# Kernel optimization log

Hardware: AMD Instinct MI355X
Metric: run time of the kernel (lower is better)

Reference implementation:

```python
import jax, jax.numpy as jnp
import numpy as np

BETA = 0.25
COMMIT_W = 1.0
EPS = 1e-6
N_E, E_DIM, C = 8192, 256, 256
B, H, W = 16, 32, 32


def setup_inputs() -> dict:
    key = jax.random.key(0)
    k1, k2, k3 = jax.random.split(key, 3)
    z = jax.random.normal(k1, (B, C, H, W), jnp.float32)
    frozen_codebook = jax.random.normal(k2, (N_E, E_DIM), jnp.float32) * (E_DIM ** -0.5)
    w_transform = jax.random.normal(k3, (C, E_DIM), jnp.float32) * (E_DIM ** -0.5)
    return {"z": z, "frozen_codebook": frozen_codebook, "w_transform": w_transform}


def _rotate_to(src, tgt):
    # Rotation trick: Householder-style rotation of src onto direction of tgt.
    sg = jax.lax.stop_gradient
    norm_src = jnp.linalg.norm(src, axis=-1, keepdims=True)
    norm_tgt = jnp.linalg.norm(tgt, axis=-1, keepdims=True)
    u = src / jnp.clip(norm_src, EPS)          # normalized source
    q = tgt / jnp.clip(norm_tgt, EPS)          # normalized target
    w = u + q
    w = sg(w / jnp.clip(jnp.linalg.norm(w, axis=-1, keepdims=True), EPS))
    u = sg(u)
    q = sg(q)
    e = src  # gradients flow through e only (rotation matrix is detached)
    rotated = (e
               - 2.0 * jnp.sum(e * w, axis=-1, keepdims=True) * w
               + 2.0 * jnp.sum(e * u, axis=-1, keepdims=True) * q)
    return rotated * sg(norm_tgt / jnp.clip(norm_src, EPS))


def reference(z, frozen_codebook, w_transform):
    z = z.astype(jnp.float32)
    zc = jnp.transpose(z, (0, 2, 3, 1))          # b h w c
    z_flat = zc.reshape(-1, zc.shape[-1])        # [N, C]
    codebook = frozen_codebook @ w_transform.T   # [n_e, C] (Linear, no bias)

    # squared L2 distances, argmin under no_grad
    d = (jnp.sum(z_flat ** 2, axis=1, keepdims=True)
         + jnp.sum(codebook ** 2, axis=1)
         - 2.0 * jnp.einsum('bd,nd->bn', z_flat, codebook))
    indices = jnp.argmin(jax.lax.stop_gradient(d), axis=1)  # [N]

    z_q_flat = codebook[indices]                 # [N, C]
    sg = jax.lax.stop_gradient
    loss = (jnp.mean((sg(z_flat) - z_q_flat) ** 2)
            + BETA * jnp.mean((z_flat - sg(z_q_flat)) ** 2)) * COMMIT_W

    z_q_flat = _rotate_to(z_flat, z_q_flat)      # rotation trick
    z_q = z_q_flat.reshape(zc.shape)             # b h w c
    z_q = jnp.transpose(z_q, (0, 3, 1, 2))       # b c h w
    return z_q, loss, indices
```

## Files before the change

kernel.cpp:

```cpp
#include <hip/hip_runtime.h>
#include <math.h>

typedef unsigned short u16;
typedef unsigned int   u32;

#define B_   16
#define C_   256
#define HW_  1024
#define N_   16384
#define NE_  8192
#define K_   256
#define NSPLIT 8
#define CPS  1024
#define NZQ  4194304

typedef _Float16 f16x8 __attribute__((ext_vector_type(8)));
typedef float    f32x16 __attribute__((ext_vector_type(16)));


__device__ __forceinline__ u16 f2h(float x) {
    union { _Float16 h; u16 u; } c;
    c.h = (_Float16)x;
    return c.u;
}

__global__ void k_transpose_z(const float* __restrict__ z, float* __restrict__ zf,
                              u16* __restrict__ zh) {
    __shared__ float tile[32][33];
    int b   = blockIdx.z;
    int hw0 = blockIdx.x * 32;
    int c0  = blockIdx.y * 32;
    int tx = threadIdx.x;
    int ty = threadIdx.y;
    #pragma unroll
    for (int i = 0; i < 4; ++i) {
        int c = c0 + ty + i * 8;
        tile[ty + i * 8][tx] = z[((size_t)b * C_ + c) * HW_ + hw0 + tx];
    }
    __syncthreads();
    #pragma unroll
    for (int i = 0; i < 4; ++i) {
        int hw = hw0 + ty + i * 8;
        size_t o = ((size_t)b * HW_ + hw) * C_ + c0 + tx;
        float v = tile[tx][ty + i * 8];
        zf[o] = v;
        zh[o] = f2h(v);
    }
}

__global__ __launch_bounds__(256) void k_codebook_gemm(
        const float* __restrict__ f, const float* __restrict__ w,
        float* __restrict__ cb, u16* __restrict__ cbh) {
    __shared__ float Fs[16][68];
    __shared__ float Ws[16][68];
    int n0 = blockIdx.x * 64;
    int c0 = blockIdx.y * 64;
    int tid = threadIdx.x;
    int tx = tid & 15, ty = tid >> 4;
    int nl = tid >> 2;
    int kq = (tid & 3) * 4;
    float acc[4][4] = {};
    for (int kb = 0; kb < K_; kb += 16) {
        float4 fv = *(const float4*)&f[(size_t)(n0 + nl) * K_ + kb + kq];
        float4 wv = *(const float4*)&w[(size_t)(c0 + nl) * K_ + kb + kq];
        __syncthreads();
        Fs[kq + 0][nl] = fv.x; Fs[kq + 1][nl] = fv.y; Fs[kq + 2][nl] = fv.z; Fs[kq + 3][nl] = fv.w;
        Ws[kq + 0][nl] = wv.x; Ws[kq + 1][nl] = wv.y; Ws[kq + 2][nl] = wv.z; Ws[kq + 3][nl] = wv.w;
        __syncthreads();
        #pragma unroll
        for (int k = 0; k < 16; ++k) {
            float4 a = *(float4*)&Fs[k][ty * 4];
            float4 b = *(float4*)&Ws[k][tx * 4];
            float av[4] = {a.x, a.y, a.z, a.w};
            float bv[4] = {b.x, b.y, b.z, b.w};
            #pragma unroll
            for (int i = 0; i < 4; ++i)
                #pragma unroll
                for (int j = 0; j < 4; ++j)
                    acc[i][j] += av[i] * bv[j];
        }
    }
    #pragma unroll
    for (int i = 0; i < 4; ++i) {
        size_t o = (size_t)(n0 + ty * 4 + i) * K_ + c0 + tx * 4;
        *(float4*)&cb[o] = make_float4(acc[i][0], acc[i][1], acc[i][2], acc[i][3]);
        *(ushort4*)&cbh[o] = make_ushort4(f2h(acc[i][0]), f2h(acc[i][1]),
                                          f2h(acc[i][2]), f2h(acc[i][3]));
    }
}

__global__ void k_c2(const float* __restrict__ cb, float* __restrict__ c2,
                     double* __restrict__ c2d) {
    int row  = blockIdx.x * 4 + (threadIdx.x >> 6);
    int lane = threadIdx.x & 63;
    float4 v = *(const float4*)&cb[(size_t)row * K_ + lane * 4];
    double s = (double)v.x * v.x + (double)v.y * v.y
             + (double)v.z * v.z + (double)v.w * v.w;
    #pragma unroll
    for (int off = 32; off; off >>= 1) s += __shfl_down(s, off, 64);
    if (lane == 0) { c2d[row] = s; c2[row] = (float)(s * 4096.0 + 262144.0); }
}

__device__ __forceinline__ void ld_lds16(const void* g, void* l) {
    __builtin_amdgcn_global_load_lds((const __attribute__((address_space(1))) void*)g,
                                     (__attribute__((address_space(3))) void*)l, 16, 0, 0);
}

#define INS(M1, M2, U) { u32 t_ = min(M1, U); u32 h_ = max(M1, U); M1 = t_; M2 = min(M2, h_); }

#define SCORE16(ACC, M1, M2, CGBASE, C2B) do {                                    \
    u32 ib_ = (u32)(code0 + (CGBASE));                                            \
    _Pragma("unroll")                                                             \
    for (int h = 0; h < 4; ++h) {                                                 \
        float4 cv = *(const float4*)&(C2B)[(CGBASE) + 8 * h];                     \
        u32 u0 = (((u32)fmaf(-8192.f, (ACC)[4*h+0], cv.x)) << 13) + ib_ + 8*h + 0; \
        u32 u1 = (((u32)fmaf(-8192.f, (ACC)[4*h+1], cv.y)) << 13) + ib_ + 8*h + 1; \
        u32 u2 = (((u32)fmaf(-8192.f, (ACC)[4*h+2], cv.z)) << 13) + ib_ + 8*h + 2; \
        u32 u3 = (((u32)fmaf(-8192.f, (ACC)[4*h+3], cv.w)) << 13) + ib_ + 8*h + 3; \
        INS(M1, M2, u0); INS(M1, M2, u1); INS(M1, M2, u2); INS(M1, M2, u3);       \
    }                                                                             \
} while (0)

#define WAITVM(N) { asm volatile("s_waitcnt vmcnt(" #N ")" ::: "memory"); \
                    __builtin_amdgcn_s_barrier();                          \
                    __builtin_amdgcn_sched_barrier(0); }

__global__ __launch_bounds__(256, 2) void k_scan_mfma(
        const u16* __restrict__ zh, const u16* __restrict__ cbh,
        const float* __restrict__ c2, int* __restrict__ t2i) {
    __shared__ __align__(16) u16 sA[4][8192];
    __shared__ __align__(16) float c2s[1024];

    int r0    = blockIdx.x * 128;
    int split = blockIdx.y;
    int tid  = threadIdx.x;
    int wave = tid >> 6, lane = tid & 63;
    int l31 = lane & 31, q = lane >> 5;
    int ra = ((wave & 1) << 6) + l31;

    const u16* zp = zh + (size_t)(r0 + ((wave >> 1) << 6) + l31) * K_ + q * 8;
    f16x8 zr0[16], zr1[16];
    #pragma unroll
    for (int t = 0; t < 16; ++t) {
        zr0[t] = *(const f16x8*)&zp[t * 16];
        zr1[t] = *(const f16x8*)&zp[32 * K_ + t * 16];
    }

    size_t ga[4]; u32 la[4];
    #pragma unroll
    for (int it = 0; it < 4; ++it) {
        int S = (it * 4 + wave) * 64 + lane;
        int row = S >> 3, u = S & 7;
        ga[it] = (size_t)row * K_ + (u ^ (row & 7)) * 8;
        la[it] = (u32)(it * 4 + wave) * 512;
    }

    u32 m1a = 0xFFFFFFFFu, m2a = 0xFFFFFFFFu;
    u32 m1b = 0xFFFFFFFFu, m2b = 0xFFFFFFFFu;

    const u16* cb0 = cbh + (size_t)split * CPS * K_;

    auto STAGE = [&](int s) {
        const u16* Ab = cb0 + (size_t)(s >> 2) * (128 * K_) + (s & 3) * 64;
        u16* d = &sA[s & 3][0];
        #pragma unroll
        for (int it = 0; it < 4; ++it) ld_lds16(Ab + ga[it], d + la[it]);
    };

    f32x16 acc0 = (f32x16){}, acc1 = (f32x16){}, acc2 = (f32x16){}, acc3 = (f32x16){};

    auto COMPUTE = [&](int ct, int kb) {
        const u16* sAb = &sA[kb][0];
        __builtin_amdgcn_s_setprio(1);
        #pragma unroll
        for (int ks = 0; ks < 4; ++ks) {
            u32 u8 = (u32)(((ks * 2 + q) ^ (l31 & 7)) * 8);
            f16x8 af0 = *(const f16x8*)&sAb[(u32)ra * 64 + u8];
            f16x8 af1 = *(const f16x8*)&sAb[(u32)ra * 64 + 2048 + u8];
            acc0 = __builtin_amdgcn_mfma_f32_32x32x16_f16(af0, zr0[kb * 4 + ks], acc0, 0, 0, 0);
            acc1 = __builtin_amdgcn_mfma_f32_32x32x16_f16(af1, zr0[kb * 4 + ks], acc1, 0, 0, 0);
            acc2 = __builtin_amdgcn_mfma_f32_32x32x16_f16(af0, zr1[kb * 4 + ks], acc2, 0, 0, 0);
            acc3 = __builtin_amdgcn_mfma_f32_32x32x16_f16(af1, zr1[kb * 4 + ks], acc3, 0, 0, 0);
        }
        __builtin_amdgcn_s_setprio(0);
        if (kb == 3) {
            int code0 = split * CPS + ct * 128;
            const float* C2B = &c2s[ct * 128];
            int cga = ((wave & 1) << 6) + (q << 2);
            int cgb = cga + 32;
            SCORE16(acc0, m1a, m2a, cga, C2B);
            SCORE16(acc1, m1a, m2a, cgb, C2B);
            SCORE16(acc2, m1b, m2b, cga, C2B);
            SCORE16(acc3, m1b, m2b, cgb, C2B);
            acc0 = (f32x16){}; acc1 = (f32x16){}; acc2 = (f32x16){}; acc3 = (f32x16){};
        }
    };

    STAGE(0); STAGE(1);
    ld_lds16(&c2[split * CPS + wave * 256 + lane * 4], &c2s[wave * 256]);
    asm volatile("s_waitcnt vmcnt(0)" ::: "memory");
    __builtin_amdgcn_s_barrier();
    __builtin_amdgcn_sched_barrier(0);

    for (int ct = 0; ct < 7; ++ct) {
        #pragma unroll
        for (int kb = 0; kb < 4; ++kb) {
            STAGE(ct * 4 + kb + 2);
            WAITVM(8);
            COMPUTE(ct, kb);
        }
    }
    STAGE(30); WAITVM(8); COMPUTE(7, 0);
    STAGE(31); WAITVM(8); COMPUTE(7, 1);
    WAITVM(4);            COMPUTE(7, 2);
    WAITVM(0);            COMPUTE(7, 3);

    {
        u32 o1 = __shfl_xor(m1a, 32, 64), o2 = __shfl_xor(m2a, 32, 64);
        u32 h = max(m1a, o1); m1a = min(m1a, o1); m2a = min(min(m2a, o2), h);
        o1 = __shfl_xor(m1b, 32, 64); o2 = __shfl_xor(m2b, 32, 64);
        h = max(m1b, o1); m1b = min(m1b, o1); m2b = min(min(m2b, o2), h);
    }
    u32* mbuf = (u32*)&sA[0][0];
    if (q == 0) {
        int base = ((wave * 2 + 0) * 32 + l31) * 2;
        mbuf[base] = m1a; mbuf[base + 1] = m2a;
        base = ((wave * 2 + 1) * 32 + l31) * 2;
        mbuf[base] = m1b; mbuf[base + 1] = m2b;
    }
    __syncthreads();
    if (tid < 128) {
        int zr = tid, wp = zr >> 6, zg = (zr >> 5) & 1, l = zr & 31;
        int iA = (((wp * 2 + 0) * 2 + zg) * 32 + l) * 2;
        int iB = (((wp * 2 + 1) * 2 + zg) * 32 + l) * 2;
        u32 a1 = mbuf[iA], a2 = mbuf[iA + 1];
        u32 b1 = mbuf[iB], b2 = mbuf[iB + 1];
        u32 h  = max(a1, b1), f1 = min(a1, b1);
        u32 f2 = min(min(a2, b2), h);
        size_t o = ((size_t)split * N_ + (r0 + zr)) * 2;
        t2i[o] = (int)(f1 & 0x1FFFu);
        t2i[o + 1] = (int)(f2 & 0x1FFFu);
    }
}

__global__ __launch_bounds__(256) void k_finalize(
        const float* __restrict__ zf, const float* __restrict__ cb,
        const double* __restrict__ c2d, const int* __restrict__ t2i,
        float* __restrict__ out, float* __restrict__ partials) {
    __shared__ int   bidx[16];
    __shared__ float wsum[4];
    __shared__ float tile[16][260];
    int n0 = blockIdx.x * 16;
    int tid = threadIdx.x;
    int wv = tid >> 6, lane = tid & 63;
    int h = lane >> 5, l5 = lane & 31;

    for (int rr = 0; rr < 4; ++rr) {
        int n = n0 + wv * 4 + rr;
        double bs = 1e300; int bi = 0x7fffffff;
        for (int p = 0; p < 8; ++p) {
            int t = 2 * p + h;
            int sp = t >> 1, wsel = t & 1;
            int ci = t2i[((size_t)sp * N_ + n) * 2 + wsel];
            double acc = 0.0;
            const float* zp = zf + (size_t)n * K_;
            const float* cp = cb + (size_t)ci * K_;
            #pragma unroll
            for (int jj = 0; jj < 2; ++jj) {
                float4 zv = *(const float4*)&zp[l5 * 4 + jj * 128];
                float4 cv = *(const float4*)&cp[l5 * 4 + jj * 128];
                acc += (double)zv.x * cv.x + (double)zv.y * cv.y
                     + (double)zv.z * cv.z + (double)zv.w * cv.w;
            }
            #pragma unroll
            for (int off = 1; off < 32; off <<= 1) acc += __shfl_xor(acc, off, 32);
            double sc = c2d[ci] - 2.0 * acc;
            double so = __shfl_xor(sc, 32, 64);
            int    io = __shfl_xor(ci, 32, 64);
            double s0 = h ? so : sc;  int i0 = h ? io : ci;
            double s1 = h ? sc : so;  int i1 = h ? ci : io;
            if (s0 < bs || (s0 == bs && i0 < bi)) { bs = s0; bi = i0; }
            if (s1 < bs || (s1 == bs && i1 < bi)) { bs = s1; bi = i1; }
        }
        if (lane == 0) {
            bidx[wv * 4 + rr] = bi;
            out[(size_t)NZQ + 1 + n] = (float)bi;
        }
    }
    __syncthreads();

    float accl = 0.f;
    for (int l = 0; l < 16; ++l) {
        int n = n0 + l;
        int bi = bidx[l];
        float zq = cb[(size_t)bi * K_ + tid];
        float d  = zf[(size_t)n * K_ + tid] - zq;
        accl += d * d;
        tile[l][tid] = zq;
    }
    #pragma unroll
    for (int off = 32; off; off >>= 1) accl += __shfl_down(accl, off, 64);
    if ((tid & 63) == 0) wsum[tid >> 6] = accl;
    __syncthreads();
    if (tid == 0) partials[blockIdx.x] = wsum[0] + wsum[1] + wsum[2] + wsum[3];
    int b = n0 >> 10, hw0 = n0 & 1023;
    #pragma unroll
    for (int g = 0; g < 4; ++g) {
        float4 v = make_float4(tile[g * 4 + 0][tid], tile[g * 4 + 1][tid],
                               tile[g * 4 + 2][tid], tile[g * 4 + 3][tid]);
        *(float4*)&out[((size_t)b * C_ + tid) * HW_ + hw0 + g * 4] = v;
    }
}

__global__ void k_loss(const float* __restrict__ partials, float* __restrict__ out) {
    __shared__ double ws4[4];
    int tid = threadIdx.x;
    double s = 0.0;
    for (int i = tid; i < 1024; i += 256) s += (double)partials[i];
    #pragma unroll
    for (int off = 32; off; off >>= 1) s += __shfl_down(s, off, 64);
    if ((tid & 63) == 0) ws4[tid >> 6] = s;
    __syncthreads();
    if (tid == 0) {
        double tot = ws4[0] + ws4[1] + ws4[2] + ws4[3];
        out[NZQ] = (float)(1.25 * tot / (double)NZQ);
    }
}

extern "C" void kernel_launch(void* const* d_in, const int* in_sizes, int n_in,
                              void* d_out, int out_size, void* d_ws, size_t ws_size,
                              hipStream_t stream) {
    const float* z  = (const float*)d_in[0];
    const float* fc = (const float*)d_in[1];
    const float* wt = (const float*)d_in[2];
    float* out = (float*)d_out;

    float* ws = (float*)d_ws;
    const size_t OFF_ZF   = 0;
    const size_t OFF_CB   = OFF_ZF + (size_t)N_ * K_;
    const size_t OFF_C2   = OFF_CB + (size_t)NE_ * K_;
    const size_t OFF_C2D  = OFF_C2 + NE_;
    const size_t OFF_T2I  = OFF_C2D + (size_t)NE_ * 2;
    const size_t OFF_PART = OFF_T2I + (size_t)NSPLIT * N_ * 2;
    const size_t OFF_ZH   = OFF_PART + 1024;
    const size_t OFF_CBH  = OFF_ZH + (size_t)N_ * K_ / 2;

    float*  zf   = ws + OFF_ZF;
    float*  cb   = ws + OFF_CB;
    float*  c2   = ws + OFF_C2;
    double* c2d  = (double*)(ws + OFF_C2D);
    int*    t2i  = (int*)(ws + OFF_T2I);
    float*  part = ws + OFF_PART;
    u16*    zh   = (u16*)(ws + OFF_ZH);
    u16*    cbh  = (u16*)(ws + OFF_CBH);

    k_transpose_z<<<dim3(HW_ / 32, C_ / 32, B_), dim3(32, 8), 0, stream>>>(z, zf, zh);
    k_codebook_gemm<<<dim3(NE_ / 64, K_ / 64), 256, 0, stream>>>(fc, wt, cb, cbh);
    k_c2<<<NE_ / 4, 256, 0, stream>>>(cb, c2, c2d);
    k_scan_mfma<<<dim3(N_ / 128, NSPLIT), 256, 0, stream>>>(zh, cbh, c2, t2i);
    k_finalize<<<N_ / 16, 256, 0, stream>>>(zf, cb, c2d, t2i, out, part);
    k_loss<<<1, 256, 0, stream>>>(part, out);
}
```

Before: 224.3 us.

## Give each wave private double-buffered LDS tiles to drop per-stage block barriers

Each wave now stages its own codebook slice into a private LDS double buffer instead of sharing a four-slot block-wide buffer. This removes the block barrier in every pipeline step, so waves only wait on their own vmcnt. The cost is that waves sharing the same codebook rows (wave pairs with equal wave&1) now load them twice, doubling global and L2 traffic. The prefetch depth also drops from two stages to one, which may expose more load latency.

```diff
diff --git a/kernel.cpp b/kernel.cpp
--- a/kernel.cpp
+++ b/kernel.cpp
@@ -121,14 +121,10 @@
     }                                                                             \
 } while (0)
 
-#define WAITVM(N) { asm volatile("s_waitcnt vmcnt(" #N ")" ::: "memory"); \
-                    __builtin_amdgcn_s_barrier();                          \
-                    __builtin_amdgcn_sched_barrier(0); }
-
 __global__ __launch_bounds__(256, 2) void k_scan_mfma(
         const u16* __restrict__ zh, const u16* __restrict__ cbh,
         const float* __restrict__ c2, int* __restrict__ t2i) {
-    __shared__ __align__(16) u16 sA[4][8192];
+    __shared__ __align__(16) u16 sW[4][2][4096];
     __shared__ __align__(16) float c2s[1024];
 
     int r0    = blockIdx.x * 128;
@@ -136,7 +132,6 @@
     int tid  = threadIdx.x;
     int wave = tid >> 6, lane = tid & 63;
     int l31 = lane & 31, q = lane >> 5;
-    int ra = ((wave & 1) << 6) + l31;
 
     const u16* zp = zh + (size_t)(r0 + ((wave >> 1) << 6) + l31) * K_ + q * 8;
     f16x8 zr0[16], zr1[16];
@@ -146,37 +141,36 @@
         zr1[t] = *(const f16x8*)&zp[32 * K_ + t * 16];
     }
 
-    size_t ga[4]; u32 la[4];
-    #pragma unroll
-    for (int it = 0; it < 4; ++it) {
-        int S = (it * 4 + wave) * 64 + lane;
-        int row = S >> 3, u = S & 7;
-        ga[it] = (size_t)row * K_ + (u ^ (row & 7)) * 8;
-        la[it] = (u32)(it * 4 + wave) * 512;
+    u32 go[8];
+    #pragma unroll
+    for (int j = 0; j < 8; ++j) {
+        int idx = j * 64 + lane;
+        int r = idx >> 3, u = idx & 7;
+        go[j] = (u32)r * 256 + (u32)((u ^ (r & 7)) * 8);
     }
 
     u32 m1a = 0xFFFFFFFFu, m2a = 0xFFFFFFFFu;
     u32 m1b = 0xFFFFFFFFu, m2b = 0xFFFFFFFFu;
 
-    const u16* cb0 = cbh + (size_t)split * CPS * K_;
+    const u16* cbW = cbh + ((size_t)split * CPS + ((wave & 1) << 6)) * K_;
 
     auto STAGE = [&](int s) {
-        const u16* Ab = cb0 + (size_t)(s >> 2) * (128 * K_) + (s & 3) * 64;
-        u16* d = &sA[s & 3][0];
+        const u16* Ab = cbW + (size_t)(s >> 2) * (128 * K_) + (s & 3) * 64;
+        u16* d = &sW[wave][s & 1][0];
         #pragma unroll
-        for (int it = 0; it < 4; ++it) ld_lds16(Ab + ga[it], d + la[it]);
+        for (int j = 0; j < 8; ++j) ld_lds16(Ab + go[j], d + j * 512);
     };
 
     f32x16 acc0 = (f32x16){}, acc1 = (f32x16){}, acc2 = (f32x16){}, acc3 = (f32x16){};
 
     auto COMPUTE = [&](int ct, int kb) {
-        const u16* sAb = &sA[kb][0];
+        const u16* sAb = &sW[wave][kb & 1][0];
         __builtin_amdgcn_s_setprio(1);
         #pragma unroll
         for (int ks = 0; ks < 4; ++ks) {
             u32 u8 = (u32)(((ks * 2 + q) ^ (l31 & 7)) * 8);
-            f16x8 af0 = *(const f16x8*)&sAb[(u32)ra * 64 + u8];
-            f16x8 af1 = *(const f16x8*)&sAb[(u32)ra * 64 + 2048 + u8];
+            f16x8 af0 = *(const f16x8*)&sAb[(u32)l31 * 64 + u8];
+            f16x8 af1 = *(const f16x8*)&sAb[(u32)l31 * 64 + 2048 + u8];
             acc0 = __builtin_amdgcn_mfma_f32_32x32x16_f16(af0, zr0[kb * 4 + ks], acc0, 0, 0, 0);
             acc1 = __builtin_amdgcn_mfma_f32_32x32x16_f16(af1, zr0[kb * 4 + ks], acc1, 0, 0, 0);
             acc2 = __builtin_amdgcn_mfma_f32_32x32x16_f16(af0, zr1[kb * 4 + ks], acc2, 0, 0, 0);
@@ -196,24 +190,24 @@
         }
     };
 
-    STAGE(0); STAGE(1);
+    STAGE(0);
     ld_lds16(&c2[split * CPS + wave * 256 + lane * 4], &c2s[wave * 256]);
     asm volatile("s_waitcnt vmcnt(0)" ::: "memory");
-    __builtin_amdgcn_s_barrier();
-    __builtin_amdgcn_sched_barrier(0);
-
-    for (int ct = 0; ct < 7; ++ct) {
+    __syncthreads();
+
+    for (int ct = 0; ct < 8; ++ct) {
         #pragma unroll
         for (int kb = 0; kb < 4; ++kb) {
-            STAGE(ct * 4 + kb + 2);
-            WAITVM(8);
+            int s = ct * 4 + kb;
+            if (s < 31) {
+                STAGE(s + 1);
+                asm volatile("s_waitcnt vmcnt(8)" ::: "memory");
+            } else {
+                asm volatile("s_waitcnt vmcnt(0)" ::: "memory");
+            }
             COMPUTE(ct, kb);
         }
     }
-    STAGE(30); WAITVM(8); COMPUTE(7, 0);
-    STAGE(31); WAITVM(8); COMPUTE(7, 1);
-    WAITVM(4);            COMPUTE(7, 2);
-    WAITVM(0);            COMPUTE(7, 3);
 
     {
         u32 o1 = __shfl_xor(m1a, 32, 64), o2 = __shfl_xor(m2a, 32, 64);
@@ -221,7 +215,8 @@
         o1 = __shfl_xor(m1b, 32, 64); o2 = __shfl_xor(m2b, 32, 64);
         h = max(m1b, o1); m1b = min(m1b, o1); m2b = min(min(m2b, o2), h);
     }
-    u32* mbuf = (u32*)&sA[0][0];
+    __syncthreads();
+    u32* mbuf = (u32*)&sW[0][0][0];
     if (q == 0) {
         int base = ((wave * 2 + 0) * 32 + l31) * 2;
         mbuf[base] = m1a; mbuf[base + 1] = m2a;
```

Result: slower. 235.8 us (+5.2%).

## Halve codebook splits in scan and prefetch loads in GEMM and finalize

Applied to the files above, without the earlier changes.

The MFMA scan kernel now covers 2048 codes per block with 4 splits instead of 1024 codes with 8, so fewer candidate pairs are written and the finalize pass rescores 8 candidates per row instead of 16. The codebook GEMM prefetches the next k-slice into registers before the inner product loop, and finalize loads the z row once and software-pipelines the codebook row loads. The tradeoff is half as many blocks in the scan grid, which reduces parallelism and latency hiding, plus a larger c2 LDS buffer.

```diff
diff --git a/kernel.cpp b/kernel.cpp
--- a/kernel.cpp
+++ b/kernel.cpp
@@ -10,8 +10,8 @@
 #define N_   16384
 #define NE_  8192
 #define K_   256
-#define NSPLIT 8
-#define CPS  1024
+#define NSPLIT 4
+#define CPS  2048
 #define NZQ  4194304
 
 typedef _Float16 f16x8 __attribute__((ext_vector_type(8)));
@@ -60,13 +60,17 @@
     int nl = tid >> 2;
     int kq = (tid & 3) * 4;
     float acc[4][4] = {};
+    float4 fv = *(const float4*)&f[(size_t)(n0 + nl) * K_ + kq];
+    float4 wv = *(const float4*)&w[(size_t)(c0 + nl) * K_ + kq];
     for (int kb = 0; kb < K_; kb += 16) {
-        float4 fv = *(const float4*)&f[(size_t)(n0 + nl) * K_ + kb + kq];
-        float4 wv = *(const float4*)&w[(size_t)(c0 + nl) * K_ + kb + kq];
         __syncthreads();
         Fs[kq + 0][nl] = fv.x; Fs[kq + 1][nl] = fv.y; Fs[kq + 2][nl] = fv.z; Fs[kq + 3][nl] = fv.w;
         Ws[kq + 0][nl] = wv.x; Ws[kq + 1][nl] = wv.y; Ws[kq + 2][nl] = wv.z; Ws[kq + 3][nl] = wv.w;
         __syncthreads();
+        if (kb + 16 < K_) {
+            fv = *(const float4*)&f[(size_t)(n0 + nl) * K_ + kb + 16 + kq];
+            wv = *(const float4*)&w[(size_t)(c0 + nl) * K_ + kb + 16 + kq];
+        }
         #pragma unroll
         for (int k = 0; k < 16; ++k) {
             float4 a = *(float4*)&Fs[k][ty * 4];
@@ -129,7 +133,7 @@
         const u16* __restrict__ zh, const u16* __restrict__ cbh,
         const float* __restrict__ c2, int* __restrict__ t2i) {
     __shared__ __align__(16) u16 sA[4][8192];
-    __shared__ __align__(16) float c2s[1024];
+    __shared__ __align__(16) float c2s[2048];
 
     int r0    = blockIdx.x * 128;
     int split = blockIdx.y;
@@ -197,12 +201,13 @@
     };
 
     STAGE(0); STAGE(1);
-    ld_lds16(&c2[split * CPS + wave * 256 + lane * 4], &c2s[wave * 256]);
+    ld_lds16(&c2[split * CPS + wave * 512 + lane * 4], &c2s[wave * 512]);
+    ld_lds16(&c2[split * CPS + wave * 512 + 256 + lane * 4], &c2s[wave * 512 + 256]);
     asm volatile("s_waitcnt vmcnt(0)" ::: "memory");
     __builtin_amdgcn_s_barrier();
     __builtin_amdgcn_sched_barrier(0);
 
-    for (int ct = 0; ct < 7; ++ct) {
+    for (int ct = 0; ct < 15; ++ct) {
         #pragma unroll
         for (int kb = 0; kb < 4; ++kb) {
             STAGE(ct * 4 + kb + 2);
@@ -210,10 +215,10 @@
             COMPUTE(ct, kb);
         }
     }
-    STAGE(30); WAITVM(8); COMPUTE(7, 0);
-    STAGE(31); WAITVM(8); COMPUTE(7, 1);
-    WAITVM(4);            COMPUTE(7, 2);
-    WAITVM(0);            COMPUTE(7, 3);
+    STAGE(62); WAITVM(8); COMPUTE(15, 0);
+    STAGE(63); WAITVM(8); COMPUTE(15, 1);
+    WAITVM(4);            COMPUTE(15, 2);
+    WAITVM(0);            COMPUTE(15, 3);
 
     {
         u32 o1 = __shfl_xor(m1a, 32, 64), o2 = __shfl_xor(m2a, 32, 64);
@@ -257,24 +262,35 @@
 
     for (int rr = 0; rr < 4; ++rr) {
         int n = n0 + wv * 4 + rr;
+        const float* zp = zf + (size_t)n * K_;
+        float4 za = *(const float4*)&zp[l5 * 4];
+        float4 zb = *(const float4*)&zp[l5 * 4 + 128];
+        int cid[4];
+        #pragma unroll
+        for (int p = 0; p < 4; ++p)
+            cid[p] = t2i[((size_t)p * N_ + n) * 2 + h];
+        double c2p[4];
+        #pragma unroll
+        for (int p = 0; p < 4; ++p) c2p[p] = c2d[cid[p]];
+        float4 cva = *(const float4*)&cb[(size_t)cid[0] * K_ + l5 * 4];
+        float4 cvb = *(const float4*)&cb[(size_t)cid[0] * K_ + l5 * 4 + 128];
+
         double bs = 1e300; int bi = 0x7fffffff;
-        for (int p = 0; p < 8; ++p) {
-            int t = 2 * p + h;
-            int sp = t >> 1, wsel = t & 1;
-            int ci = t2i[((size_t)sp * N_ + n) * 2 + wsel];
-            double acc = 0.0;
-            const float* zp = zf + (size_t)n * K_;
-            const float* cp = cb + (size_t)ci * K_;
-            #pragma unroll
-            for (int jj = 0; jj < 2; ++jj) {
-                float4 zv = *(const float4*)&zp[l5 * 4 + jj * 128];
-                float4 cv = *(const float4*)&cp[l5 * 4 + jj * 128];
-                acc += (double)zv.x * cv.x + (double)zv.y * cv.y
-                     + (double)zv.z * cv.z + (double)zv.w * cv.w;
+        #pragma unroll
+        for (int p = 0; p < 4; ++p) {
+            float4 ca = cva, cbv = cvb;
+            if (p < 3) {
+                cva = *(const float4*)&cb[(size_t)cid[p + 1] * K_ + l5 * 4];
+                cvb = *(const float4*)&cb[(size_t)cid[p + 1] * K_ + l5 * 4 + 128];
             }
+            double acc = (double)za.x * ca.x + (double)za.y * ca.y
+                       + (double)za.z * ca.z + (double)za.w * ca.w
+                       + (double)zb.x * cbv.x + (double)zb.y * cbv.y
+                       + (double)zb.z * cbv.z + (double)zb.w * cbv.w;
             #pragma unroll
             for (int off = 1; off < 32; off <<= 1) acc += __shfl_xor(acc, off, 32);
-            double sc = c2d[ci] - 2.0 * acc;
+            double sc = c2p[p] - 2.0 * acc;
+            int    ci = cid[p];
             double so = __shfl_xor(sc, 32, 64);
             int    io = __shfl_xor(ci, 32, 64);
             double s0 = h ? so : sc;  int i0 = h ? io : ci;
```

New measurement: 201.9 us. 1.11x faster.
